# Kernel optimization log

Measured on AMD Instinct MI355X. Metric: run time of the kernel, lower is better.

The kernel has to match this reference:

```python
import jax, jax.numpy as jnp
import numpy as np

D_MODEL = 1024
NUM_HEADS = 16
HEAD_DIM = D_MODEL // NUM_HEADS


def setup_inputs() -> dict:
    key = jax.random.key(0)
    ks = jax.random.split(key, 5)
    B, S = 4, 2048
    scale = 0.02
    return {
        "x": jax.random.normal(ks[0], (B, S, D_MODEL), dtype=jnp.float32),
        "q_proj_weight": jax.random.normal(ks[1], (D_MODEL, D_MODEL), dtype=jnp.float32) * scale,
        "k_proj_weight": jax.random.normal(ks[2], (D_MODEL, D_MODEL), dtype=jnp.float32) * scale,
        "v_proj_weight": jax.random.normal(ks[3], (D_MODEL, D_MODEL), dtype=jnp.float32) * scale,
        "o_proj_weight": jax.random.normal(ks[4], (D_MODEL, D_MODEL), dtype=jnp.float32) * scale,
    }


def reference(x, q_proj_weight, k_proj_weight, v_proj_weight, o_proj_weight):
    B, S, _ = x.shape
    H, Dh = NUM_HEADS, HEAD_DIM

    def proj(w):  # [B,S,d_model] x [d_k,d_in] -> [B,H,S,Dh]
        p = jnp.einsum('bsd,kd->bsk', x, w)
        return p.reshape(B, S, H, Dh).transpose(0, 2, 1, 3)

    q = proj(q_proj_weight)
    k = proj(k_proj_weight)
    v = proj(v_proj_weight)

    scores = jnp.einsum('bhqd,bhkd->bhqk', q, k) / jnp.sqrt(jnp.asarray(Dh, dtype=x.dtype))
    causal = jnp.tril(jnp.ones((S, S), dtype=bool))  # [S,S]
    scores = jnp.where(causal, scores, -jnp.inf)
    attn = jax.nn.softmax(scores, axis=-1)
    out = jnp.einsum('bhqk,bhkd->bhqd', attn, v)  # [B,H,S,Dh]
    out = out.transpose(0, 2, 1, 3).reshape(B, S, D_MODEL)
    return jnp.einsum('bsv,mv->bsm', out, o_proj_weight)
```

## Files before the change

kernel.cpp:

```cpp
#include <hip/hip_runtime.h>
#include <cstdint>
#include <cstddef>

#define NH 16
#define DH 64
#define SEQ 2048
#define DM 1024

typedef __attribute__((ext_vector_type(8))) short short8;
typedef __attribute__((ext_vector_type(4))) float f32x4;

__device__ __forceinline__ unsigned short f2bf(float f) {
  unsigned u = __builtin_bit_cast(unsigned, f);
  u += 0x7fffu + ((u >> 16) & 1u);
  return (unsigned short)(u >> 16);
}

__device__ __forceinline__ void gld_lds16(const void* g, void* l) {
  __builtin_amdgcn_global_load_lds((const __attribute__((address_space(1))) void*)g,
                                   (__attribute__((address_space(3))) void*)l,
                                   16, 0, 0);
}

__global__ __launch_bounds__(256) void cast_all_kernel(const float* __restrict__ x,
                                                       const float* __restrict__ wq,
                                                       const float* __restrict__ wk,
                                                       const float* __restrict__ wv,
                                                       const float* __restrict__ wo,
                                                       unsigned short* __restrict__ xb,
                                                       unsigned short* __restrict__ wqkvb,
                                                       unsigned short* __restrict__ wob) {
  const int bid = blockIdx.x;
  const float* in;
  unsigned short* out;
  int i;
  if (bid < 8192) {
    in = x; out = xb; i = bid * 256 + threadIdx.x;
  } else {
    const int w = (bid - 8192) >> 10;
    i = ((bid - 8192) & 1023) * 256 + threadIdx.x;
    in = (w == 0) ? wq : (w == 1) ? wk : (w == 2) ? wv : wo;
    out = (w < 3) ? (wqkvb + (size_t)w * 1048576) : wob;
  }
  const float4 v = ((const float4*)in)[i];
  ushort4 o;
  o.x = f2bf(v.x); o.y = f2bf(v.y); o.z = f2bf(v.z); o.w = f2bf(v.w);
  ((ushort4*)out)[i] = o;
}

__global__ __launch_bounds__(256, 4) void gemm_qkv(const unsigned short* __restrict__ A,
                                                   const unsigned short* __restrict__ W,
                                                   unsigned short* __restrict__ qb,
                                                   unsigned short* __restrict__ kb,
                                                   unsigned short* __restrict__ vtb) {
  __shared__ __align__(16) unsigned short As[128 * 32];
  __shared__ __align__(16) unsigned short Bs[128 * 32];
  const int t = threadIdx.x;
  const int lane = t & 63;
  const int wave = t >> 6;
  const int quad = lane >> 4;
  const int l16 = lane & 15;
  const int wm = (wave >> 1) * 64;
  const int wn = (wave & 1) * 64;

  const int lid = blockIdx.x + 24 * blockIdx.y;
  const int xcd = lid & 7;
  const int idx = lid >> 3;
  const int bm = (xcd * 8 + idx / 24) * 128;
  const int bn = (idx % 24) * 128;
  const int sel = bn >> 10;
  const int bnl = bn & 1023;

  f32x4 acc[4][4];
#pragma unroll
  for (int i = 0; i < 4; ++i)
#pragma unroll
    for (int j = 0; j < 4; ++j) acc[i][j] = {0.0f, 0.0f, 0.0f, 0.0f};

  const int srow = t >> 2;
  const int sc = (t & 3) ^ ((srow >> 1) & 3);
  const unsigned short* Ag1 = A + (size_t)(bm + srow) * DM + sc * 8;
  const unsigned short* Ag2 = A + (size_t)(bm + srow + 64) * DM + sc * 8;
  const unsigned short* Bg1 = W + (size_t)(bn + srow) * DM + sc * 8;
  const unsigned short* Bg2 = W + (size_t)(bn + srow + 64) * DM + sc * 8;
  const int swz = (l16 >> 1) & 3;

  for (int k0 = 0; k0 < DM; k0 += 32) {
    __syncthreads();
    gld_lds16(Ag1 + k0, As + t * 8);
    gld_lds16(Ag2 + k0, As + t * 8 + 2048);
    gld_lds16(Bg1 + k0, Bs + t * 8);
    gld_lds16(Bg2 + k0, Bs + t * 8 + 2048);
    __syncthreads();
    short8 af[4], bfr[4];
#pragma unroll
    for (int i = 0; i < 4; ++i)
      af[i] = *(const short8*)(As + (wm + i * 16 + l16) * 32 + ((quad ^ swz) * 8));
#pragma unroll
    for (int j = 0; j < 4; ++j)
      bfr[j] = *(const short8*)(Bs + (wn + j * 16 + l16) * 32 + ((quad ^ swz) * 8));
#pragma unroll
    for (int i = 0; i < 4; ++i)
#pragma unroll
      for (int j = 0; j < 4; ++j)
        acc[i][j] = __builtin_amdgcn_mfma_f32_16x16x32_bf16(af[i], bfr[j], acc[i][j], 0, 0, 0);
  }

#pragma unroll
  for (int i = 0; i < 4; ++i) {
#pragma unroll
    for (int j = 0; j < 4; ++j) {
#pragma unroll
      for (int r = 0; r < 4; ++r) {
        const int m = bm + wm + i * 16 + quad * 4 + r;
        const int n = bnl + wn + j * 16 + l16;
        const float v = acc[i][j][r];
        if (sel == 0) {
          qb[(size_t)m * DM + n] = f2bf(v * 0.125f);
        } else if (sel == 1) {
          kb[(size_t)m * DM + n] = f2bf(v);
        } else {
          const int bb = m >> 11, s = m & 2047;
          const int h = n >> 6, d = n & 63;
          vtb[((size_t)((bb * NH + h) * DH + d)) * SEQ + s] = f2bf(v);
        }
      }
    }
  }
}

__global__ __launch_bounds__(256, 4) void gemm_o(const unsigned short* __restrict__ A,
                                                 const unsigned short* __restrict__ B,
                                                 float* __restrict__ C) {
  __shared__ __align__(16) unsigned short As[128 * 32];
  __shared__ __align__(16) unsigned short Bs[128 * 32];
  const int t = threadIdx.x;
  const int lane = t & 63;
  const int wave = t >> 6;
  const int quad = lane >> 4;
  const int l16 = lane & 15;
  const int wm = (wave >> 1) * 64;
  const int wn = (wave & 1) * 64;

  const int lid = blockIdx.x + 8 * blockIdx.y;
  const int xcd = lid & 7;
  const int idx = lid >> 3;
  const int bm = (xcd * 8 + idx / 8) * 128;
  const int bn = (idx % 8) * 128;

  f32x4 acc[4][4];
#pragma unroll
  for (int i = 0; i < 4; ++i)
#pragma unroll
    for (int j = 0; j < 4; ++j) acc[i][j] = {0.0f, 0.0f, 0.0f, 0.0f};

  const int srow = t >> 2;
  const int sc = (t & 3) ^ ((srow >> 1) & 3);
  const unsigned short* Ag1 = A + (size_t)(bm + srow) * DM + sc * 8;
  const unsigned short* Ag2 = A + (size_t)(bm + srow + 64) * DM + sc * 8;
  const unsigned short* Bg1 = B + (size_t)(bn + srow) * DM + sc * 8;
  const unsigned short* Bg2 = B + (size_t)(bn + srow + 64) * DM + sc * 8;
  const int swz = (l16 >> 1) & 3;

  for (int k0 = 0; k0 < DM; k0 += 32) {
    __syncthreads();
    gld_lds16(Ag1 + k0, As + t * 8);
    gld_lds16(Ag2 + k0, As + t * 8 + 2048);
    gld_lds16(Bg1 + k0, Bs + t * 8);
    gld_lds16(Bg2 + k0, Bs + t * 8 + 2048);
    __syncthreads();
    short8 af[4], bfr[4];
#pragma unroll
    for (int i = 0; i < 4; ++i)
      af[i] = *(const short8*)(As + (wm + i * 16 + l16) * 32 + ((quad ^ swz) * 8));
#pragma unroll
    for (int j = 0; j < 4; ++j)
      bfr[j] = *(const short8*)(Bs + (wn + j * 16 + l16) * 32 + ((quad ^ swz) * 8));
#pragma unroll
    for (int i = 0; i < 4; ++i)
#pragma unroll
      for (int j = 0; j < 4; ++j)
        acc[i][j] = __builtin_amdgcn_mfma_f32_16x16x32_bf16(af[i], bfr[j], acc[i][j], 0, 0, 0);
  }

#pragma unroll
  for (int i = 0; i < 4; ++i)
#pragma unroll
    for (int j = 0; j < 4; ++j)
#pragma unroll
      for (int r = 0; r < 4; ++r) {
        const int m = bm + wm + i * 16 + quad * 4 + r;
        const int n = bn + wn + j * 16 + l16;
        C[(size_t)m * DM + n] = acc[i][j][r];
      }
}

__global__ __launch_bounds__(512) void attn_kernel(const unsigned short* __restrict__ Q,
                                                   const unsigned short* __restrict__ K,
                                                   const unsigned short* __restrict__ Vt,
                                                   unsigned short* __restrict__ O) {
  __shared__ __align__(16) unsigned short Ks[128 * 64];
  __shared__ __align__(16) unsigned short Vs[64 * 128];
  __shared__ __align__(16) unsigned short Ps[8][16 * 136];
  const int t = threadIdx.x;
  const int lane = t & 63;
  const int wave = t >> 6;
  const int quad = lane >> 4;
  const int l16 = lane & 15;
  const int h = blockIdx.y;
  const int b = blockIdx.z;

  const int ksr1 = t >> 3;
  const int ksr2 = (t + 512) >> 3;
  const int koff1 = (b * SEQ + ksr1) * DM + h * 64 + (((t & 7) ^ (ksr1 & 7)) * 8);
  const int koff2 = (b * SEQ + ksr2) * DM + h * 64 + (((t & 7) ^ (ksr2 & 7)) * 8);
  const int vsr1 = t >> 4;
  const int vsr2 = (t + 512) >> 4;
  const int voff1 = ((b * NH + h) * DH + vsr1) * SEQ + (((t & 15) ^ (vsr1 & 15)) * 8);
  const int voff2 = ((b * NH + h) * DH + vsr2) * SEQ + (((t & 15) ^ (vsr2 & 15)) * 8);
  unsigned short* Pw = &Ps[wave][0];
  const int swz = l16 & 7;

#pragma unroll 1
  for (int pass = 0; pass < 2; ++pass) {
    const int qt = (pass == 0) ? (int)blockIdx.x : 15 - (int)blockIdx.x;
    const int qtile = qt * 128;
    const int row_lo = qtile + wave * 16;
    const int row_hi = row_lo + 15;

    const unsigned short* Qrow =
        Q + ((size_t)(b * SEQ + row_lo + l16)) * DM + h * 64;
    const short8 qf0 = *(const short8*)(Qrow + quad * 8);
    const short8 qf1 = *(const short8*)(Qrow + 32 + quad * 8);

    f32x4 o_acc[4];
#pragma unroll
    for (int nb = 0; nb < 4; ++nb) o_acc[nb] = {0.0f, 0.0f, 0.0f, 0.0f};
    float l_r[4] = {0.0f, 0.0f, 0.0f, 0.0f};

    const int ktiles = qt + 1;
    for (int kt = 0; kt < ktiles; ++kt) {
      const int kbase = kt * 128;
      __syncthreads();
      gld_lds16(K + koff1 + (size_t)kbase * DM, Ks + t * 8);
      gld_lds16(K + koff2 + (size_t)kbase * DM, Ks + (t + 512) * 8);
      gld_lds16(Vt + voff1 + kbase, Vs + t * 8);
      gld_lds16(Vt + voff2 + kbase, Vs + (t + 512) * 8);
      __syncthreads();

      if (kbase <= row_hi) {
        f32x4 s_acc[8];
#pragma unroll
        for (int nb = 0; nb < 8; ++nb) {
          s_acc[nb] = {0.0f, 0.0f, 0.0f, 0.0f};
          const short8 kf0 = *(const short8*)(Ks + (nb * 16 + l16) * 64 + ((quad ^ swz) * 8));
          const short8 kf1 = *(const short8*)(Ks + (nb * 16 + l16) * 64 + (((4 | quad) ^ swz) * 8));
          s_acc[nb] = __builtin_amdgcn_mfma_f32_16x16x32_bf16(qf0, kf0, s_acc[nb], 0, 0, 0);
          s_acc[nb] = __builtin_amdgcn_mfma_f32_16x16x32_bf16(qf1, kf1, s_acc[nb], 0, 0, 0);
        }

        const bool need_mask = (kbase + 127 > row_lo);
#pragma unroll
        for (int r = 0; r < 4; ++r) {
          const int qr = row_lo + quad * 4 + r;
#pragma unroll
          for (int nb = 0; nb < 8; ++nb) {
            float p = __expf(s_acc[nb][r]);
            if (need_mask) p = ((kbase + nb * 16 + l16) <= qr) ? p : 0.0f;
            l_r[r] += p;
            const unsigned u = __builtin_bit_cast(unsigned, p);
            Pw[(quad * 4 + r) * 136 + nb * 16 + l16] =
                (unsigned short)((u + 0x8000u) >> 16);
          }
        }

#pragma unroll
        for (int kk = 0; kk < 4; ++kk) {
          const short8 pf = *(const short8*)(Pw + l16 * 136 + kk * 32 + quad * 8);
#pragma unroll
          for (int nb = 0; nb < 4; ++nb) {
            const short8 vf = *(const short8*)(Vs + (nb * 16 + l16) * 128 +
                                               (((kk * 4 + quad) ^ l16) * 8));
            o_acc[nb] = __builtin_amdgcn_mfma_f32_16x16x32_bf16(pf, vf, o_acc[nb], 0, 0, 0);
          }
        }
      }
    }

#pragma unroll
    for (int r = 0; r < 4; ++r) {
      float ls = l_r[r];
      ls += __shfl_xor(ls, 1);
      ls += __shfl_xor(ls, 2);
      ls += __shfl_xor(ls, 4);
      ls += __shfl_xor(ls, 8);
      const float inv_l = 1.0f / ls;
      const int qr = row_lo + quad * 4 + r;
#pragma unroll
      for (int nb = 0; nb < 4; ++nb)
        O[((size_t)(b * SEQ + qr)) * DM + h * 64 + nb * 16 + l16] =
            f2bf(o_acc[nb][r] * inv_l);
    }
  }
}

extern "C" void kernel_launch(void* const* d_in, const int* in_sizes, int n_in,
                              void* d_out, int out_size, void* d_ws, size_t ws_size,
                              hipStream_t stream) {
  const float* x  = (const float*)d_in[0];
  const float* wq = (const float*)d_in[1];
  const float* wk = (const float*)d_in[2];
  const float* wv = (const float*)d_in[3];
  const float* wo = (const float*)d_in[4];

  char* ws = (char*)d_ws;
  unsigned short* xb    = (unsigned short*)(ws);
  unsigned short* wqkvb = (unsigned short*)(ws + 16777216);
  unsigned short* wob   = (unsigned short*)(ws + 23068672);
  unsigned short* qb    = (unsigned short*)(ws + 25165824);
  unsigned short* kb    = (unsigned short*)(ws + 41943040);
  unsigned short* vtb   = (unsigned short*)(ws + 58720256);
  unsigned short* aob   = (unsigned short*)(ws + 75497472);

  cast_all_kernel<<<12288, 256, 0, stream>>>(x, wq, wk, wv, wo, xb, wqkvb, wob);

  gemm_qkv<<<dim3(24, 64), 256, 0, stream>>>(xb, wqkvb, qb, kb, vtb);

  attn_kernel<<<dim3(8, NH, 4), 512, 0, stream>>>(qb, kb, vtb, aob);

  gemm_o<<<dim3(8, 64), 256, 0, stream>>>(aob, wob, (float*)d_out);
}
```

Measured before the change: 269.9 us.

## Fuse cast, QKV GEMM, attention and O GEMM into one persistent kernel

Replaces the four separate launches with a single persistent kernel of 512 blocks that runs the cast, QKV projection, causal attention and output projection in phases. Atomic-counter grid barriers separate the phases, removing launch gaps and tail effects between kernels. The GEMM phases now use 128x128 tiles with 8 waves each computing 64x32, and the XCD-aware tile remapping is dropped from the fallback kernels. The grid barrier relies on all 512 blocks being co-resident and adds a memset, and the attention phase keeps the fixed 8x16x4 work mapping.

```diff
diff --git a/kernel.cpp b/kernel.cpp
--- a/kernel.cpp
+++ b/kernel.cpp
@@ -20,6 +20,283 @@
   __builtin_amdgcn_global_load_lds((const __attribute__((address_space(1))) void*)g,
                                    (__attribute__((address_space(3))) void*)l,
                                    16, 0, 0);
+}
+
+__device__ __forceinline__ void grid_bar(unsigned* cnt, unsigned target) {
+  __syncthreads();
+  if (threadIdx.x == 0) {
+    __hip_atomic_fetch_add(cnt, 1u, __ATOMIC_ACQ_REL, __HIP_MEMORY_SCOPE_AGENT);
+    while (__hip_atomic_load(cnt, __ATOMIC_ACQUIRE, __HIP_MEMORY_SCOPE_AGENT) < target)
+      __builtin_amdgcn_s_sleep(8);
+  }
+  __syncthreads();
+}
+
+__global__ __launch_bounds__(512, 4) void fused_mha(
+    const float* __restrict__ x, const float* __restrict__ wq,
+    const float* __restrict__ wk, const float* __restrict__ wv,
+    const float* __restrict__ wo,
+    unsigned short* __restrict__ xb, unsigned short* __restrict__ wqkvb,
+    unsigned short* __restrict__ wob, unsigned short* __restrict__ qb,
+    unsigned short* __restrict__ kb, unsigned short* __restrict__ vtb,
+    unsigned short* __restrict__ aob, float* __restrict__ dout,
+    unsigned* __restrict__ bars) {
+  __shared__ __align__(16) unsigned short smem[33792];
+  const int t = threadIdx.x;
+  const int bid = blockIdx.x;
+  const int lane = t & 63;
+  const int wave = t >> 6;
+  const int quad = (lane >> 4) & 3;
+  const int l16 = lane & 15;
+  const unsigned nblk = gridDim.x;
+
+  {
+    const int gtid = bid * 512 + t;
+#pragma unroll 1
+    for (int it = 0; it < 12; ++it) {
+      const int idx = it * 262144 + gtid;
+      if (idx < 2097152) {
+        const float4 v = ((const float4*)x)[idx];
+        ushort4 o;
+        o.x = f2bf(v.x); o.y = f2bf(v.y); o.z = f2bf(v.z); o.w = f2bf(v.w);
+        ((ushort4*)xb)[idx] = o;
+      } else {
+        const int widx = idx - 2097152;
+        const int w = widx >> 18;
+        const int off = widx & 262143;
+        const float4* src =
+            (const float4*)(w == 0 ? wq : w == 1 ? wk : w == 2 ? wv : wo);
+        ushort4* dst = (w < 3) ? ((ushort4*)wqkvb + (size_t)w * 262144)
+                               : (ushort4*)wob;
+        const float4 v = src[off];
+        ushort4 o;
+        o.x = f2bf(v.x); o.y = f2bf(v.y); o.z = f2bf(v.z); o.w = f2bf(v.w);
+        dst[off] = o;
+      }
+    }
+  }
+  grid_bar(bars + 0, nblk);
+
+  {
+    unsigned short* As = smem;
+    unsigned short* Bs = smem + 4096;
+    const int wm = (wave >> 2) * 64;
+    const int wn = (wave & 3) * 32;
+    const int srow = t >> 2;
+    const int sc = (t & 3) ^ ((srow >> 1) & 3);
+    const int swz = (l16 >> 1) & 3;
+#pragma unroll 1
+    for (int tl = 0; tl < 3; ++tl) {
+      const int tid = tl * 512 + bid;
+      const int bm = (tid / 24) * 128;
+      const int bnf = (tid % 24) * 128;
+      const int sel = bnf >> 10;
+      const int bnl = bnf & 1023;
+      const unsigned short* Ag = xb + (size_t)(bm + srow) * DM + sc * 8;
+      const unsigned short* Bg = wqkvb + (size_t)(bnf + srow) * DM + sc * 8;
+
+      f32x4 acc[4][2];
+#pragma unroll
+      for (int i = 0; i < 4; ++i)
+#pragma unroll
+        for (int j = 0; j < 2; ++j) acc[i][j] = {0.0f, 0.0f, 0.0f, 0.0f};
+
+      for (int k0 = 0; k0 < DM; k0 += 32) {
+        __syncthreads();
+        gld_lds16(Ag + k0, As + t * 8);
+        gld_lds16(Bg + k0, Bs + t * 8);
+        __syncthreads();
+        short8 af[4], bfr[2];
+#pragma unroll
+        for (int i = 0; i < 4; ++i)
+          af[i] = *(const short8*)(As + (wm + i * 16 + l16) * 32 + ((quad ^ swz) * 8));
+#pragma unroll
+        for (int j = 0; j < 2; ++j)
+          bfr[j] = *(const short8*)(Bs + (wn + j * 16 + l16) * 32 + ((quad ^ swz) * 8));
+#pragma unroll
+        for (int i = 0; i < 4; ++i)
+#pragma unroll
+          for (int j = 0; j < 2; ++j)
+            acc[i][j] = __builtin_amdgcn_mfma_f32_16x16x32_bf16(af[i], bfr[j], acc[i][j], 0, 0, 0);
+      }
+
+#pragma unroll
+      for (int i = 0; i < 4; ++i) {
+#pragma unroll
+        for (int j = 0; j < 2; ++j) {
+#pragma unroll
+          for (int r = 0; r < 4; ++r) {
+            const int m = bm + wm + i * 16 + quad * 4 + r;
+            const int n = bnl + wn + j * 16 + l16;
+            const float v = acc[i][j][r];
+            if (sel == 0) {
+              qb[(size_t)m * DM + n] = f2bf(v * 0.125f);
+            } else if (sel == 1) {
+              kb[(size_t)m * DM + n] = f2bf(v);
+            } else {
+              const int bb = m >> 11, s = m & 2047;
+              const int hh = n >> 6, d = n & 63;
+              vtb[((size_t)((bb * NH + hh) * DH + d)) * SEQ + s] = f2bf(v);
+            }
+          }
+        }
+      }
+    }
+  }
+  grid_bar(bars + 1, nblk);
+
+  {
+    unsigned short* Ks = smem;
+    unsigned short* Vs = smem + 8192;
+    unsigned short* Ps = smem + 16384;
+    const int bx = bid & 7;
+    const int h = (bid >> 3) & 15;
+    const int b = bid >> 7;
+
+    const int ksr1 = t >> 3;
+    const int ksr2 = (t + 512) >> 3;
+    const int koff1 = (b * SEQ + ksr1) * DM + h * 64 + (((t & 7) ^ (ksr1 & 7)) * 8);
+    const int koff2 = (b * SEQ + ksr2) * DM + h * 64 + (((t & 7) ^ (ksr2 & 7)) * 8);
+    const int vsr1 = t >> 4;
+    const int vsr2 = (t + 512) >> 4;
+    const int voff1 = ((b * NH + h) * DH + vsr1) * SEQ + (((t & 15) ^ (vsr1 & 15)) * 8);
+    const int voff2 = ((b * NH + h) * DH + vsr2) * SEQ + (((t & 15) ^ (vsr2 & 15)) * 8);
+    unsigned short* Pw = Ps + wave * 2176;
+    const int swz8 = l16 & 7;
+
+#pragma unroll 1
+    for (int pass = 0; pass < 2; ++pass) {
+      const int qt = (pass == 0) ? bx : 15 - bx;
+      const int qtile = qt * 128;
+      const int row_lo = qtile + wave * 16;
+      const int row_hi = row_lo + 15;
+
+      const unsigned short* Qrow =
+          qb + ((size_t)(b * SEQ + row_lo + l16)) * DM + h * 64;
+      const short8 qf0 = *(const short8*)(Qrow + quad * 8);
+      const short8 qf1 = *(const short8*)(Qrow + 32 + quad * 8);
+
+      f32x4 o_acc[4];
+#pragma unroll
+      for (int nb = 0; nb < 4; ++nb) o_acc[nb] = {0.0f, 0.0f, 0.0f, 0.0f};
+      float l_r[4] = {0.0f, 0.0f, 0.0f, 0.0f};
+
+      const int ktiles = qt + 1;
+      for (int kt = 0; kt < ktiles; ++kt) {
+        const int kbase = kt * 128;
+        __syncthreads();
+        gld_lds16(kb + koff1 + (size_t)kbase * DM, Ks + t * 8);
+        gld_lds16(kb + koff2 + (size_t)kbase * DM, Ks + (t + 512) * 8);
+        gld_lds16(vtb + voff1 + kbase, Vs + t * 8);
+        gld_lds16(vtb + voff2 + kbase, Vs + (t + 512) * 8);
+        __syncthreads();
+
+        if (kbase <= row_hi) {
+          f32x4 s_acc[8];
+#pragma unroll
+          for (int nb = 0; nb < 8; ++nb) {
+            s_acc[nb] = {0.0f, 0.0f, 0.0f, 0.0f};
+            const short8 kf0 = *(const short8*)(Ks + (nb * 16 + l16) * 64 + ((quad ^ swz8) * 8));
+            const short8 kf1 = *(const short8*)(Ks + (nb * 16 + l16) * 64 + (((4 | quad) ^ swz8) * 8));
+            s_acc[nb] = __builtin_amdgcn_mfma_f32_16x16x32_bf16(qf0, kf0, s_acc[nb], 0, 0, 0);
+            s_acc[nb] = __builtin_amdgcn_mfma_f32_16x16x32_bf16(qf1, kf1, s_acc[nb], 0, 0, 0);
+          }
+
+          const bool need_mask = (kbase + 127 > row_lo);
+#pragma unroll
+          for (int r = 0; r < 4; ++r) {
+            const int qr = row_lo + quad * 4 + r;
+#pragma unroll
+            for (int nb = 0; nb < 8; ++nb) {
+              float p = __expf(s_acc[nb][r]);
+              if (need_mask) p = ((kbase + nb * 16 + l16) <= qr) ? p : 0.0f;
+              l_r[r] += p;
+              const unsigned u = __builtin_bit_cast(unsigned, p);
+              Pw[(quad * 4 + r) * 136 + nb * 16 + l16] =
+                  (unsigned short)((u + 0x8000u) >> 16);
+            }
+          }
+
+#pragma unroll
+          for (int kk = 0; kk < 4; ++kk) {
+            const short8 pf = *(const short8*)(Pw + l16 * 136 + kk * 32 + quad * 8);
+#pragma unroll
+            for (int nb = 0; nb < 4; ++nb) {
+              const short8 vf = *(const short8*)(Vs + (nb * 16 + l16) * 128 +
+                                                 (((kk * 4 + quad) ^ l16) * 8));
+              o_acc[nb] = __builtin_amdgcn_mfma_f32_16x16x32_bf16(pf, vf, o_acc[nb], 0, 0, 0);
+            }
+          }
+        }
+      }
+
+#pragma unroll
+      for (int r = 0; r < 4; ++r) {
+        float ls = l_r[r];
+        ls += __shfl_xor(ls, 1);
+        ls += __shfl_xor(ls, 2);
+        ls += __shfl_xor(ls, 4);
+        ls += __shfl_xor(ls, 8);
+        const float inv_l = 1.0f / ls;
+        const int qr = row_lo + quad * 4 + r;
+#pragma unroll
+        for (int nb = 0; nb < 4; ++nb)
+          aob[((size_t)(b * SEQ + qr)) * DM + h * 64 + nb * 16 + l16] =
+              f2bf(o_acc[nb][r] * inv_l);
+      }
+    }
+  }
+  grid_bar(bars + 2, nblk);
+
+  {
+    unsigned short* As = smem;
+    unsigned short* Bs = smem + 4096;
+    const int wm = (wave >> 2) * 64;
+    const int wn = (wave & 3) * 32;
+    const int srow = t >> 2;
+    const int sc = (t & 3) ^ ((srow >> 1) & 3);
+    const int swz = (l16 >> 1) & 3;
+    const int bm = (bid >> 3) * 128;
+    const int bn = (bid & 7) * 128;
+    const unsigned short* Ag = aob + (size_t)(bm + srow) * DM + sc * 8;
+    const unsigned short* Bg = wob + (size_t)(bn + srow) * DM + sc * 8;
+
+    f32x4 acc[4][2];
+#pragma unroll
+    for (int i = 0; i < 4; ++i)
+#pragma unroll
+      for (int j = 0; j < 2; ++j) acc[i][j] = {0.0f, 0.0f, 0.0f, 0.0f};
+
+    for (int k0 = 0; k0 < DM; k0 += 32) {
+      __syncthreads();
+      gld_lds16(Ag + k0, As + t * 8);
+      gld_lds16(Bg + k0, Bs + t * 8);
+      __syncthreads();
+      short8 af[4], bfr[2];
+#pragma unroll
+      for (int i = 0; i < 4; ++i)
+        af[i] = *(const short8*)(As + (wm + i * 16 + l16) * 32 + ((quad ^ swz) * 8));
+#pragma unroll
+      for (int j = 0; j < 2; ++j)
+        bfr[j] = *(const short8*)(Bs + (wn + j * 16 + l16) * 32 + ((quad ^ swz) * 8));
+#pragma unroll
+      for (int i = 0; i < 4; ++i)
+#pragma unroll
+        for (int j = 0; j < 2; ++j)
+          acc[i][j] = __builtin_amdgcn_mfma_f32_16x16x32_bf16(af[i], bfr[j], acc[i][j], 0, 0, 0);
+    }
+
+#pragma unroll
+    for (int i = 0; i < 4; ++i)
+#pragma unroll
+      for (int j = 0; j < 2; ++j)
+#pragma unroll
+        for (int r = 0; r < 4; ++r) {
+          const int m = bm + wm + i * 16 + quad * 4 + r;
+          const int n = bn + wn + j * 16 + l16;
+          dout[(size_t)m * DM + n] = acc[i][j][r];
+        }
+  }
 }
 
 __global__ __launch_bounds__(256) void cast_all_kernel(const float* __restrict__ x,
@@ -62,12 +339,8 @@
   const int l16 = lane & 15;
   const int wm = (wave >> 1) * 64;
   const int wn = (wave & 1) * 64;
-
-  const int lid = blockIdx.x + 24 * blockIdx.y;
-  const int xcd = lid & 7;
-  const int idx = lid >> 3;
-  const int bm = (xcd * 8 + idx / 24) * 128;
-  const int bn = (idx % 24) * 128;
+  const int bm = blockIdx.y * 128;
+  const int bn = blockIdx.x * 128;
   const int sel = bn >> 10;
   const int bnl = bn & 1023;
 
@@ -141,12 +414,8 @@
   const int l16 = lane & 15;
   const int wm = (wave >> 1) * 64;
   const int wn = (wave & 1) * 64;
-
-  const int lid = blockIdx.x + 8 * blockIdx.y;
-  const int xcd = lid & 7;
-  const int idx = lid >> 3;
-  const int bm = (xcd * 8 + idx / 8) * 128;
-  const int bn = (idx % 8) * 128;
+  const int bm = blockIdx.y * 128;
+  const int bn = blockIdx.x * 128;
 
   f32x4 acc[4][4];
 #pragma unroll
@@ -219,7 +488,7 @@
   const int voff1 = ((b * NH + h) * DH + vsr1) * SEQ + (((t & 15) ^ (vsr1 & 15)) * 8);
   const int voff2 = ((b * NH + h) * DH + vsr2) * SEQ + (((t & 15) ^ (vsr2 & 15)) * 8);
   unsigned short* Pw = &Ps[wave][0];
-  const int swz = l16 & 7;
+  const int swz8 = l16 & 7;
 
 #pragma unroll 1
   for (int pass = 0; pass < 2; ++pass) {
@@ -253,8 +522,8 @@
 #pragma unroll
         for (int nb = 0; nb < 8; ++nb) {
           s_acc[nb] = {0.0f, 0.0f, 0.0f, 0.0f};
-          const short8 kf0 = *(const short8*)(Ks + (nb * 16 + l16) * 64 + ((quad ^ swz) * 8));
-          const short8 kf1 = *(const short8*)(Ks + (nb * 16 + l16) * 64 + (((4 | quad) ^ swz) * 8));
+          const short8 kf0 = *(const short8*)(Ks + (nb * 16 + l16) * 64 + ((quad ^ swz8) * 8));
+          const short8 kf1 = *(const short8*)(Ks + (nb * 16 + l16) * 64 + (((4 | quad) ^ swz8) * 8));
           s_acc[nb] = __builtin_amdgcn_mfma_f32_16x16x32_bf16(qf0, kf0, s_acc[nb], 0, 0, 0);
           s_acc[nb] = __builtin_amdgcn_mfma_f32_16x16x32_bf16(qf1, kf1, s_acc[nb], 0, 0, 0);
         }
@@ -322,11 +591,15 @@
   unsigned short* vtb   = (unsigned short*)(ws + 58720256);
   unsigned short* aob   = (unsigned short*)(ws + 75497472);
 
-  cast_all_kernel<<<12288, 256, 0, stream>>>(x, wq, wk, wv, wo, xb, wqkvb, wob);
-
-  gemm_qkv<<<dim3(24, 64), 256, 0, stream>>>(xb, wqkvb, qb, kb, vtb);
-
-  attn_kernel<<<dim3(8, NH, 4), 512, 0, stream>>>(qb, kb, vtb, aob);
-
-  gemm_o<<<dim3(8, 64), 256, 0, stream>>>(aob, wob, (float*)d_out);
-}
+  if (ws_size >= 92274688ull + 256ull) {
+    unsigned* bars = (unsigned*)(ws + 92274688);
+    hipMemsetAsync(bars, 0, 256, stream);
+    fused_mha<<<512, 512, 0, stream>>>(x, wq, wk, wv, wo, xb, wqkvb, wob,
+                                       qb, kb, vtb, aob, (float*)d_out, bars);
+  } else {
+    cast_all_kernel<<<12288, 256, 0, stream>>>(x, wq, wk, wv, wo, xb, wqkvb, wob);
+    gemm_qkv<<<dim3(24, 64), 256, 0, stream>>>(xb, wqkvb, qb, kb, vtb);
+    attn_kernel<<<dim3(8, NH, 4), 512, 0, stream>>>(qb, kb, vtb, aob);
+    gemm_o<<<dim3(8, 64), 256, 0, stream>>>(aob, wob, (float*)d_out);
+  }
+}
```

After: 501.2 us. 1.86x slower.
